# Kernel tuning notes

Hardware: AMD Instinct MI355X
Metric: run time of the kernel (lower is better)

## Reference

```python
import jax, jax.numpy as jnp
import numpy as np


def _gcn_conv(x, edge_index, edge_weight, W, b, n_nodes):
    # PyG GCNConv with normalize=True: add self-loops (weight 1), symmetric norm,
    # transform then aggregate: out[col] += norm * (x @ W)[row], plus bias.
    row = jnp.concatenate([edge_index[0], jnp.arange(n_nodes)])
    col = jnp.concatenate([edge_index[1], jnp.arange(n_nodes)])
    w = jnp.concatenate([edge_weight, jnp.ones((n_nodes,), x.dtype)])
    deg = jax.ops.segment_sum(w, col, num_segments=n_nodes)
    dinv = jnp.where(deg > 0, jax.lax.rsqrt(jnp.maximum(deg, 1e-12)), 0.0)
    norm = dinv[row] * w * dinv[col]            # [E+N]
    h = x @ W                                   # [N, out]
    msg = h[row] * norm[:, None]                # [E+N, out]
    out = jax.ops.segment_sum(msg, col, num_segments=n_nodes)
    return out + b


def setup_inputs() -> dict:
    key = jax.random.key(0)
    ks = jax.random.split(key, 6)
    N, E, F_IN, H, C = 50000, 800000, 512, 128, 40
    features = jax.random.normal(ks[0], (N, F_IN), jnp.float32)
    edge_index = jax.random.randint(ks[1], (2, E), 0, N, jnp.int64)
    edge_weight = jax.random.uniform(ks[2], (E,), jnp.float32)
    W1 = jax.random.normal(ks[3], (F_IN, H), jnp.float32) * 0.05
    b1 = jnp.zeros((H,), jnp.float32)
    W2 = jax.random.normal(ks[4], (H, C), jnp.float32) * 0.05
    b2 = jnp.zeros((C,), jnp.float32)
    return {"features": features, "edge_index": edge_index, "edge_weight": edge_weight,
            "W1": W1, "b1": b1, "W2": W2, "b2": b2}


def reference(features, edge_index, edge_weight, W1, b1, W2, b2):
    n_nodes = features.shape[0]
    x = _gcn_conv(features, edge_index, edge_weight, W1, b1, n_nodes)
    x = jax.nn.relu(x)
    # F.dropout(training=self.training): identity in eval mode
    x = _gcn_conv(x, edge_index, edge_weight, W2, b2, n_nodes)
    return jax.nn.log_softmax(x, axis=1)
```

## Files before the change

kernel.cpp:

```cpp
#include <hip/hip_runtime.h>
#include <math.h>

#define FIN  512
#define HDIM 128
#define CDIM 40
#define CPAD 48
#define CAP  64

typedef __attribute__((ext_vector_type(8))) short shortx8;
typedef __attribute__((ext_vector_type(4))) float f32x4;

__device__ inline unsigned short f2bf(float x) {
    unsigned u = __builtin_bit_cast(unsigned, x);
    unsigned r = u + 0x7fffu + ((u >> 16) & 1u);
    return (unsigned short)(r >> 16);
}
__device__ inline float bfu(unsigned short v) { return __builtin_bit_cast(float, (unsigned)v << 16); }
__device__ inline float bflo(unsigned u) { return __builtin_bit_cast(float, u << 16); }
__device__ inline float bfhi(unsigned u) { return __builtin_bit_cast(float, u & 0xffff0000u); }
__device__ inline float asf(int i) { return __builtin_bit_cast(float, i); }
__device__ inline int   asi(float f) { return __builtin_bit_cast(int, f); }

__global__ void k_fill(const int* __restrict__ row, const int* __restrict__ col,
                       const float* __restrict__ w, int* __restrict__ cursor,
                       int2* __restrict__ bkt, int E) {
    int e = blockIdx.x * blockDim.x + threadIdx.x;
    if (e >= E) return;
    const int c = col[e];
    const int p = atomicAdd(&cursor[c], 1);
    if (p < CAP) bkt[(size_t)c * CAP + p] = make_int2(row[e], asi(w[e]));
}

__global__ __launch_bounds__(256) void k_deg(const int* __restrict__ cursor,
                                             const int2* __restrict__ bkt,
                                             float* __restrict__ dinv, int n_nodes) {
    const int node = blockIdx.x * 4 + (threadIdx.x >> 6);
    const int lane = threadIdx.x & 63;
    if (node >= n_nodes) return;
    const int cnt = min(cursor[node], CAP);
    float wsum = 0.f;
    if (lane < cnt) wsum = asf(bkt[(size_t)node * CAP + lane].y);
#pragma unroll
    for (int off = 32; off; off >>= 1) wsum += __shfl_xor(wsum, off);
    if (lane == 0) dinv[node] = rsqrtf(1.0f + wsum);
}

__global__ __launch_bounds__(256) void k_norm(const int* __restrict__ cursor,
                                              int2* __restrict__ bkt,
                                              const float* __restrict__ dinv, int n_nodes) {
    const int node = blockIdx.x * 4 + (threadIdx.x >> 6);
    const int lane = threadIdx.x & 63;
    if (node >= n_nodes) return;
    const int cnt = min(cursor[node], CAP);
    const float dl = dinv[node];
    if (lane < cnt) {
        int2 pr = bkt[(size_t)node * CAP + lane];
        pr.y = asi(asf(pr.y) * dinv[pr.x] * dl);
        bkt[(size_t)node * CAP + lane] = pr;
    }
}

__global__ void k_prepw(const float* __restrict__ W1, const float* __restrict__ W2,
                        unsigned short* __restrict__ W1T, unsigned short* __restrict__ W2T) {
    const int i = blockIdx.x * blockDim.x + threadIdx.x;
    if (i < FIN * HDIM) {
        const int k = i >> 7, n = i & 127;
        W1T[n * FIN + k] = f2bf(W1[i]);
    } else {
        const int j = i - FIN * HDIM;
        if (j < CPAD * HDIM) {
            const int n = j >> 7, k = j & 127;
            W2T[j] = (n < CDIM) ? f2bf(W2[k * CDIM + n]) : (unsigned short)0;
        }
    }
}

#define G1_LDA 72
__global__ __launch_bounds__(256) void k_gemm1(const float* __restrict__ A,
                                               const unsigned short* __restrict__ W1T,
                                               unsigned short* __restrict__ h1bf, int M) {
    __shared__ short As[128 * G1_LDA];
    __shared__ short Bs[128 * G1_LDA];
    const int tid  = threadIdx.x;
    const int wave = tid >> 6;
    const int lane = tid & 63;
    const int quad = lane >> 4;
    const int mr   = lane & 15;
    const int m0w  = (wave & 1) * 64;
    const int n0w  = (wave >> 1) * 64;
    const int m0b  = blockIdx.x * 128;

    const int srow = tid >> 1;
    const int spart = tid & 1;

    f32x4 acc[4][4];
#pragma unroll
    for (int i = 0; i < 4; i++)
#pragma unroll
        for (int j = 0; j < 4; j++) acc[i][j] = (f32x4)0.f;

    const int grow = m0b + srow;
    const bool arow_ok = grow < M;
    const float* ap = A + (size_t)grow * FIN + spart * 32;
    const unsigned short* bp = W1T + (size_t)srow * FIN + spart * 32;

    for (int k0 = 0; k0 < FIN; k0 += 64) {
#pragma unroll
        for (int i = 0; i < 4; i++) {
            float4 v0 = make_float4(0.f, 0.f, 0.f, 0.f), v1 = v0;
            if (arow_ok) {
                v0 = *(const float4*)(ap + k0 + i * 8);
                v1 = *(const float4*)(ap + k0 + i * 8 + 4);
            }
            shortx8 pk;
            pk[0] = (short)f2bf(v0.x); pk[1] = (short)f2bf(v0.y);
            pk[2] = (short)f2bf(v0.z); pk[3] = (short)f2bf(v0.w);
            pk[4] = (short)f2bf(v1.x); pk[5] = (short)f2bf(v1.y);
            pk[6] = (short)f2bf(v1.z); pk[7] = (short)f2bf(v1.w);
            *(shortx8*)&As[srow * G1_LDA + spart * 32 + i * 8] = pk;
        }
#pragma unroll
        for (int i = 0; i < 4; i++)
            *(shortx8*)&Bs[srow * G1_LDA + spart * 32 + i * 8] =
                *(const shortx8*)(bp + k0 + i * 8);
        __syncthreads();

#pragma unroll
        for (int kk = 0; kk < 2; kk++) {
            shortx8 af[4], bfr[4];
#pragma unroll
            for (int mt = 0; mt < 4; mt++)
                af[mt] = *(shortx8*)&As[(m0w + mt * 16 + mr) * G1_LDA + kk * 32 + quad * 8];
#pragma unroll
            for (int nt = 0; nt < 4; nt++)
                bfr[nt] = *(shortx8*)&Bs[(n0w + nt * 16 + mr) * G1_LDA + kk * 32 + quad * 8];
#pragma unroll
            for (int mt = 0; mt < 4; mt++)
#pragma unroll
                for (int nt = 0; nt < 4; nt++)
                    acc[mt][nt] = __builtin_amdgcn_mfma_f32_16x16x32_bf16(
                        af[mt], bfr[nt], acc[mt][nt], 0, 0, 0);
        }
        __syncthreads();
    }
#pragma unroll
    for (int mt = 0; mt < 4; mt++)
#pragma unroll
        for (int r = 0; r < 4; r++) {
            const int om = m0b + m0w + mt * 16 + quad * 4 + r;
            if (om < M) {
#pragma unroll
                for (int nt = 0; nt < 4; nt++)
                    h1bf[(size_t)om * HDIM + n0w + nt * 16 + mr] = f2bf(acc[mt][nt][r]);
            }
        }
}

__global__ __launch_bounds__(256) void k_gather1(
    const int* __restrict__ cursor, const int2* __restrict__ bkt,
    const unsigned short* __restrict__ h1bf,
    const float* __restrict__ dinv, const float* __restrict__ b1,
    unsigned short* __restrict__ x1bf, int n_nodes) {
    const int node = blockIdx.x * 4 + (threadIdx.x >> 6);
    const int lane = threadIdx.x & 63;
    if (node >= n_nodes) return;
    const int cnt = min(cursor[node], CAP);
    const int2* base = bkt + (size_t)node * CAP;
    const unsigned* h32 = (const unsigned*)h1bf;
    float a0 = 0.f, a1 = 0.f;
    int s = 0;
    for (; s + 4 <= cnt; s += 4) {
        const int4 q01 = *(const int4*)(base + s);
        const int4 q23 = *(const int4*)(base + s + 2);
        const unsigned u0 = h32[(size_t)q01.x * 64 + lane];
        const unsigned u1 = h32[(size_t)q01.z * 64 + lane];
        const unsigned u2 = h32[(size_t)q23.x * 64 + lane];
        const unsigned u3 = h32[(size_t)q23.z * 64 + lane];
        const float w0 = asf(q01.y), w1 = asf(q01.w), w2 = asf(q23.y), w3 = asf(q23.w);
        a0 += w0 * bflo(u0) + w1 * bflo(u1) + w2 * bflo(u2) + w3 * bflo(u3);
        a1 += w0 * bfhi(u0) + w1 * bfhi(u1) + w2 * bfhi(u2) + w3 * bfhi(u3);
    }
    for (; s < cnt; s++) {
        const int2 pr = base[s];
        const unsigned u = h32[(size_t)pr.x * 64 + lane];
        a0 += asf(pr.y) * bflo(u);
        a1 += asf(pr.y) * bfhi(u);
    }
    const float d = dinv[node];
    const float dd = d * d;
    const unsigned us = h32[(size_t)node * 64 + lane];
    a0 = fmaxf(a0 + dd * bflo(us) + b1[lane * 2], 0.f);
    a1 = fmaxf(a1 + dd * bfhi(us) + b1[lane * 2 + 1], 0.f);
    ((unsigned*)x1bf)[(size_t)node * 64 + lane] =
        (unsigned)f2bf(a0) | ((unsigned)f2bf(a1) << 16);
}

#define G2_LDA 136
__global__ __launch_bounds__(256) void k_gemm2(const unsigned short* __restrict__ x1bf,
                                               const unsigned short* __restrict__ W2T,
                                               unsigned short* __restrict__ h2bf, int M) {
    __shared__ short Xs[128 * G2_LDA];
    __shared__ short Ws[CPAD * G2_LDA];
    const int tid  = threadIdx.x;
    const int wave = tid >> 6;
    const int lane = tid & 63;
    const int quad = lane >> 4;
    const int mr   = lane & 15;
    const int m0b  = blockIdx.x * 128;

    {
        const int srow = tid >> 1, spart = tid & 1;
        const int grow = m0b + srow;
        if (grow < M) {
            const unsigned short* xp = x1bf + (size_t)grow * HDIM + spart * 64;
#pragma unroll
            for (int i = 0; i < 8; i++)
                *(shortx8*)&Xs[srow * G2_LDA + spart * 64 + i * 8] = *(const shortx8*)(xp + i * 8);
        } else {
#pragma unroll
            for (int i = 0; i < 8; i++)
                *(shortx8*)&Xs[srow * G2_LDA + spart * 64 + i * 8] = (shortx8)0;
        }
        for (int idx = tid; idx < CPAD * 16; idx += 256) {
            const int r = idx >> 4, j = idx & 15;
            *(shortx8*)&Ws[r * G2_LDA + j * 8] = *(const shortx8*)(W2T + r * HDIM + j * 8);
        }
    }
    __syncthreads();

    f32x4 acc[2][3];
#pragma unroll
    for (int i = 0; i < 2; i++)
#pragma unroll
        for (int j = 0; j < 3; j++) acc[i][j] = (f32x4)0.f;

    const int m0w = wave * 32;
#pragma unroll
    for (int kk = 0; kk < 4; kk++) {
        shortx8 af[2], bfr[3];
#pragma unroll
        for (int mt = 0; mt < 2; mt++)
            af[mt] = *(shortx8*)&Xs[(m0w + mt * 16 + mr) * G2_LDA + kk * 32 + quad * 8];
#pragma unroll
        for (int nt = 0; nt < 3; nt++)
            bfr[nt] = *(shortx8*)&Ws[(nt * 16 + mr) * G2_LDA + kk * 32 + quad * 8];
#pragma unroll
        for (int mt = 0; mt < 2; mt++)
#pragma unroll
            for (int nt = 0; nt < 3; nt++)
                acc[mt][nt] = __builtin_amdgcn_mfma_f32_16x16x32_bf16(
                    af[mt], bfr[nt], acc[mt][nt], 0, 0, 0);
    }
#pragma unroll
    for (int mt = 0; mt < 2; mt++)
#pragma unroll
        for (int r = 0; r < 4; r++) {
            const int om = m0b + m0w + mt * 16 + quad * 4 + r;
            if (om < M) {
#pragma unroll
                for (int nt = 0; nt < 3; nt++) {
                    const int col = nt * 16 + mr;
                    if (col < CDIM)
                        h2bf[(size_t)om * CDIM + col] = f2bf(acc[mt][nt][r]);
                }
            }
        }
}

__global__ __launch_bounds__(256) void k_gather2(
    const int* __restrict__ cursor, const int2* __restrict__ bkt,
    const unsigned short* __restrict__ h2bf,
    const float* __restrict__ dinv, const float* __restrict__ b2,
    float* __restrict__ out, int n_nodes) {
    const int node = blockIdx.x * 4 + (threadIdx.x >> 6);
    const int lane = threadIdx.x & 63;
    if (node >= n_nodes) return;
    const bool act = lane < CDIM;
    const int cnt = min(cursor[node], CAP);
    const int2* base = bkt + (size_t)node * CAP;
    float acc = 0.f;
    int s = 0;
    for (; s + 4 <= cnt; s += 4) {
        const int4 q01 = *(const int4*)(base + s);
        const int4 q23 = *(const int4*)(base + s + 2);
        if (act) {
            acc += asf(q01.y) * bfu(h2bf[(size_t)q01.x * CDIM + lane])
                 + asf(q01.w) * bfu(h2bf[(size_t)q01.z * CDIM + lane])
                 + asf(q23.y) * bfu(h2bf[(size_t)q23.x * CDIM + lane])
                 + asf(q23.w) * bfu(h2bf[(size_t)q23.z * CDIM + lane]);
        }
    }
    for (; s < cnt; s++) {
        const int2 pr = base[s];
        if (act) acc += asf(pr.y) * bfu(h2bf[(size_t)pr.x * CDIM + lane]);
    }
    if (act) {
        const float d = dinv[node];
        acc += d * d * bfu(h2bf[(size_t)node * CDIM + lane]) + b2[lane];
    }
    float m = act ? acc : -INFINITY;
#pragma unroll
    for (int off = 32; off; off >>= 1) m = fmaxf(m, __shfl_xor(m, off));
    float se = act ? expf(acc - m) : 0.f;
#pragma unroll
    for (int off = 32; off; off >>= 1) se += __shfl_xor(se, off);
    if (act) out[(size_t)node * CDIM + lane] = acc - m - logf(se);
}

extern "C" void kernel_launch(void* const* d_in, const int* in_sizes, int n_in,
                              void* d_out, int out_size, void* d_ws, size_t ws_size,
                              hipStream_t stream) {
    const float* features = (const float*)d_in[0];
    const int*   eidx     = (const int*)d_in[1];
    const float* ew       = (const float*)d_in[2];
    const float* W1       = (const float*)d_in[3];
    const float* b1       = (const float*)d_in[4];
    const float* W2       = (const float*)d_in[5];
    const float* b2       = (const float*)d_in[6];
    float* out = (float*)d_out;

    const int Nn = in_sizes[0] / FIN;
    const int E  = in_sizes[2];
    const int* row = eidx;
    const int* col = eidx + E;

    char* ws = (char*)d_ws;
    size_t off = 0;
    auto alloc = [&](size_t bytes) { void* p = ws + off; off += (bytes + 255) & ~(size_t)255; return p; };
    int*   cursor          = (int*)  alloc((size_t)Nn * 4);
    float* dinv            = (float*)alloc((size_t)Nn * 4);
    int2*  bkt             = (int2*) alloc((size_t)Nn * CAP * 8);
    unsigned short* W1T    = (unsigned short*)alloc((size_t)FIN * HDIM * 2);
    unsigned short* W2T    = (unsigned short*)alloc((size_t)CPAD * HDIM * 2);
    unsigned short* h1bf   = (unsigned short*)alloc((size_t)Nn * HDIM * 2);
    unsigned short* x1bf   = (unsigned short*)alloc((size_t)Nn * HDIM * 2);
    unsigned short* h2bf   = (unsigned short*)alloc((size_t)Nn * CDIM * 2);

    hipMemsetAsync(cursor, 0, (size_t)Nn * 4, stream);
    k_fill<<<(E + 255) / 256, 256, 0, stream>>>(row, col, ew, cursor, bkt, E);
    k_deg<<<(Nn + 3) / 4, 256, 0, stream>>>(cursor, bkt, dinv, Nn);
    k_norm<<<(Nn + 3) / 4, 256, 0, stream>>>(cursor, bkt, dinv, Nn);
    const int prep_total = FIN * HDIM + CPAD * HDIM;
    k_prepw<<<(prep_total + 255) / 256, 256, 0, stream>>>(W1, W2, W1T, W2T);
    k_gemm1<<<(Nn + 127) / 128, 256, 0, stream>>>(features, W1T, h1bf, Nn);
    k_gather1<<<(Nn + 3) / 4, 256, 0, stream>>>(cursor, bkt, h1bf, dinv, b1, x1bf, Nn);
    k_gemm2<<<(Nn + 127) / 128, 256, 0, stream>>>(x1bf, W2T, h2bf, Nn);
    k_gather2<<<(Nn + 3) / 4, 256, 0, stream>>>(cursor, bkt, h2bf, dinv, b2, out, Nn);
}
```

Before: 327.1 us.

## Fold degree normalization into GEMM epilogues and packed atomic degree accumulation

Packs the edge count and a fixed-point weight sum into one 64-bit atomic per edge, so degree comes out of the fill pass and the per-node deg and norm kernels are removed. The symmetric normalization is refactored: the source-side dinv is applied in the GEMM epilogues and the destination-side dinv once per node in the gathers, so per-edge weights stay raw. Gather loops get wider unrolling with split accumulators, and h2 rows are padded to 64 elements for aligned access. The fixed-point weight sum adds small rounding error, and the 64-bit atomics may contend more than 32-bit ones.

```diff
diff --git a/kernel.cpp b/kernel.cpp
--- a/kernel.cpp
+++ b/kernel.cpp
@@ -5,6 +5,7 @@
 #define HDIM 128
 #define CDIM 40
 #define CPAD 48
+#define H2P  64
 #define CAP  64
 
 typedef __attribute__((ext_vector_type(8))) short shortx8;
@@ -22,42 +23,28 @@
 __device__ inline int   asi(float f) { return __builtin_bit_cast(int, f); }
 
 __global__ void k_fill(const int* __restrict__ row, const int* __restrict__ col,
-                       const float* __restrict__ w, int* __restrict__ cursor,
+                       const float* __restrict__ w,
+                       unsigned long long* __restrict__ cursor,
                        int2* __restrict__ bkt, int E) {
     int e = blockIdx.x * blockDim.x + threadIdx.x;
     if (e >= E) return;
     const int c = col[e];
-    const int p = atomicAdd(&cursor[c], 1);
-    if (p < CAP) bkt[(size_t)c * CAP + p] = make_int2(row[e], asi(w[e]));
-}
-
-__global__ __launch_bounds__(256) void k_deg(const int* __restrict__ cursor,
-                                             const int2* __restrict__ bkt,
-                                             float* __restrict__ dinv, int n_nodes) {
-    const int node = blockIdx.x * 4 + (threadIdx.x >> 6);
-    const int lane = threadIdx.x & 63;
-    if (node >= n_nodes) return;
-    const int cnt = min(cursor[node], CAP);
-    float wsum = 0.f;
-    if (lane < cnt) wsum = asf(bkt[(size_t)node * CAP + lane].y);
-#pragma unroll
-    for (int off = 32; off; off >>= 1) wsum += __shfl_xor(wsum, off);
-    if (lane == 0) dinv[node] = rsqrtf(1.0f + wsum);
-}
-
-__global__ __launch_bounds__(256) void k_norm(const int* __restrict__ cursor,
-                                              int2* __restrict__ bkt,
-                                              const float* __restrict__ dinv, int n_nodes) {
-    const int node = blockIdx.x * 4 + (threadIdx.x >> 6);
-    const int lane = threadIdx.x & 63;
-    if (node >= n_nodes) return;
-    const int cnt = min(cursor[node], CAP);
-    const float dl = dinv[node];
-    if (lane < cnt) {
-        int2 pr = bkt[(size_t)node * CAP + lane];
-        pr.y = asi(asf(pr.y) * dinv[pr.x] * dl);
-        bkt[(size_t)node * CAP + lane] = pr;
-    }
+    const float we = w[e];
+    const unsigned long long wfix = (unsigned long long)(we * 4294967296.0f);
+    const unsigned long long old =
+        atomicAdd(&cursor[c], (1ULL << 40) | wfix);
+    const int p = (int)(old >> 40);
+    if (p < CAP) bkt[(size_t)c * CAP + p] = make_int2(row[e], asi(we));
+}
+
+__global__ void k_deg(const unsigned long long* __restrict__ cursor,
+                      int* __restrict__ cnt, float* __restrict__ dinv, int n) {
+    const int i = blockIdx.x * blockDim.x + threadIdx.x;
+    if (i >= n) return;
+    const unsigned long long p = cursor[i];
+    cnt[i] = min((int)(p >> 40), CAP);
+    const float wsum = (float)(p & ((1ULL << 40) - 1)) * 2.3283064365386963e-10f;
+    dinv[i] = rsqrtf(1.0f + wsum);
 }
 
 __global__ void k_prepw(const float* __restrict__ W1, const float* __restrict__ W2,
@@ -78,6 +65,7 @@
 #define G1_LDA 72
 __global__ __launch_bounds__(256) void k_gemm1(const float* __restrict__ A,
                                                const unsigned short* __restrict__ W1T,
+                                               const float* __restrict__ dinv,
                                                unsigned short* __restrict__ h1bf, int M) {
     __shared__ short As[128 * G1_LDA];
     __shared__ short Bs[128 * G1_LDA];
@@ -149,48 +137,67 @@
         for (int r = 0; r < 4; r++) {
             const int om = m0b + m0w + mt * 16 + quad * 4 + r;
             if (om < M) {
+                const float dv = dinv[om];
 #pragma unroll
                 for (int nt = 0; nt < 4; nt++)
-                    h1bf[(size_t)om * HDIM + n0w + nt * 16 + mr] = f2bf(acc[mt][nt][r]);
+                    h1bf[(size_t)om * HDIM + n0w + nt * 16 + mr] = f2bf(dv * acc[mt][nt][r]);
             }
         }
 }
 
 __global__ __launch_bounds__(256) void k_gather1(
-    const int* __restrict__ cursor, const int2* __restrict__ bkt,
+    const int* __restrict__ cnt_arr, const int2* __restrict__ bkt,
     const unsigned short* __restrict__ h1bf,
     const float* __restrict__ dinv, const float* __restrict__ b1,
     unsigned short* __restrict__ x1bf, int n_nodes) {
     const int node = blockIdx.x * 4 + (threadIdx.x >> 6);
     const int lane = threadIdx.x & 63;
     if (node >= n_nodes) return;
-    const int cnt = min(cursor[node], CAP);
+    const int cnt = cnt_arr[node];
     const int2* base = bkt + (size_t)node * CAP;
     const unsigned* h32 = (const unsigned*)h1bf;
-    float a0 = 0.f, a1 = 0.f;
+    float a0 = 0.f, a1 = 0.f, c0 = 0.f, c1 = 0.f;
     int s = 0;
-    for (; s + 4 <= cnt; s += 4) {
-        const int4 q01 = *(const int4*)(base + s);
-        const int4 q23 = *(const int4*)(base + s + 2);
-        const unsigned u0 = h32[(size_t)q01.x * 64 + lane];
-        const unsigned u1 = h32[(size_t)q01.z * 64 + lane];
-        const unsigned u2 = h32[(size_t)q23.x * 64 + lane];
-        const unsigned u3 = h32[(size_t)q23.z * 64 + lane];
-        const float w0 = asf(q01.y), w1 = asf(q01.w), w2 = asf(q23.y), w3 = asf(q23.w);
-        a0 += w0 * bflo(u0) + w1 * bflo(u1) + w2 * bflo(u2) + w3 * bflo(u3);
-        a1 += w0 * bfhi(u0) + w1 * bfhi(u1) + w2 * bfhi(u2) + w3 * bfhi(u3);
-    }
-    for (; s < cnt; s++) {
+    for (; s + 8 <= cnt; s += 8) {
+        const int4 q0 = *(const int4*)(base + s);
+        const int4 q1 = *(const int4*)(base + s + 2);
+        const int4 q2 = *(const int4*)(base + s + 4);
+        const int4 q3 = *(const int4*)(base + s + 6);
+        const unsigned u0 = h32[(size_t)q0.x * 64 + lane];
+        const unsigned u1 = h32[(size_t)q0.z * 64 + lane];
+        const unsigned u2 = h32[(size_t)q1.x * 64 + lane];
+        const unsigned u3 = h32[(size_t)q1.z * 64 + lane];
+        const unsigned u4 = h32[(size_t)q2.x * 64 + lane];
+        const unsigned u5 = h32[(size_t)q2.z * 64 + lane];
+        const unsigned u6 = h32[(size_t)q3.x * 64 + lane];
+        const unsigned u7 = h32[(size_t)q3.z * 64 + lane];
+        a0 += asf(q0.y) * bflo(u0) + asf(q0.w) * bflo(u1)
+            + asf(q1.y) * bflo(u2) + asf(q1.w) * bflo(u3);
+        a1 += asf(q0.y) * bfhi(u0) + asf(q0.w) * bfhi(u1)
+            + asf(q1.y) * bfhi(u2) + asf(q1.w) * bfhi(u3);
+        c0 += asf(q2.y) * bflo(u4) + asf(q2.w) * bflo(u5)
+            + asf(q3.y) * bflo(u6) + asf(q3.w) * bflo(u7);
+        c1 += asf(q2.y) * bfhi(u4) + asf(q2.w) * bfhi(u5)
+            + asf(q3.y) * bfhi(u6) + asf(q3.w) * bfhi(u7);
+    }
+    for (; s + 2 <= cnt; s += 2) {
+        const int4 q0 = *(const int4*)(base + s);
+        const unsigned u0 = h32[(size_t)q0.x * 64 + lane];
+        const unsigned u1 = h32[(size_t)q0.z * 64 + lane];
+        a0 += asf(q0.y) * bflo(u0) + asf(q0.w) * bflo(u1);
+        a1 += asf(q0.y) * bfhi(u0) + asf(q0.w) * bfhi(u1);
+    }
+    if (s < cnt) {
         const int2 pr = base[s];
         const unsigned u = h32[(size_t)pr.x * 64 + lane];
         a0 += asf(pr.y) * bflo(u);
         a1 += asf(pr.y) * bfhi(u);
     }
-    const float d = dinv[node];
-    const float dd = d * d;
+    a0 += c0; a1 += c1;
+    const float dl = dinv[node];
     const unsigned us = h32[(size_t)node * 64 + lane];
-    a0 = fmaxf(a0 + dd * bflo(us) + b1[lane * 2], 0.f);
-    a1 = fmaxf(a1 + dd * bfhi(us) + b1[lane * 2 + 1], 0.f);
+    a0 = fmaxf(dl * (a0 + bflo(us)) + b1[lane * 2], 0.f);
+    a1 = fmaxf(dl * (a1 + bfhi(us)) + b1[lane * 2 + 1], 0.f);
     ((unsigned*)x1bf)[(size_t)node * 64 + lane] =
         (unsigned)f2bf(a0) | ((unsigned)f2bf(a1) << 16);
 }
@@ -198,6 +205,7 @@
 #define G2_LDA 136
 __global__ __launch_bounds__(256) void k_gemm2(const unsigned short* __restrict__ x1bf,
                                                const unsigned short* __restrict__ W2T,
+                                               const float* __restrict__ dinv,
                                                unsigned short* __restrict__ h2bf, int M) {
     __shared__ short Xs[128 * G2_LDA];
     __shared__ short Ws[CPAD * G2_LDA];
@@ -257,18 +265,19 @@
         for (int r = 0; r < 4; r++) {
             const int om = m0b + m0w + mt * 16 + quad * 4 + r;
             if (om < M) {
+                const float dv = dinv[om];
 #pragma unroll
                 for (int nt = 0; nt < 3; nt++) {
                     const int col = nt * 16 + mr;
                     if (col < CDIM)
-                        h2bf[(size_t)om * CDIM + col] = f2bf(acc[mt][nt][r]);
+                        h2bf[(size_t)om * H2P + col] = f2bf(dv * acc[mt][nt][r]);
                 }
             }
         }
 }
 
 __global__ __launch_bounds__(256) void k_gather2(
-    const int* __restrict__ cursor, const int2* __restrict__ bkt,
+    const int* __restrict__ cnt_arr, const int2* __restrict__ bkt,
     const unsigned short* __restrict__ h2bf,
     const float* __restrict__ dinv, const float* __restrict__ b2,
     float* __restrict__ out, int n_nodes) {
@@ -276,27 +285,28 @@
     const int lane = threadIdx.x & 63;
     if (node >= n_nodes) return;
     const bool act = lane < CDIM;
-    const int cnt = min(cursor[node], CAP);
+    const int cnt = cnt_arr[node];
     const int2* base = bkt + (size_t)node * CAP;
-    float acc = 0.f;
+    float acc = 0.f, accb = 0.f;
     int s = 0;
     for (; s + 4 <= cnt; s += 4) {
         const int4 q01 = *(const int4*)(base + s);
         const int4 q23 = *(const int4*)(base + s + 2);
         if (act) {
-            acc += asf(q01.y) * bfu(h2bf[(size_t)q01.x * CDIM + lane])
-                 + asf(q01.w) * bfu(h2bf[(size_t)q01.z * CDIM + lane])
-                 + asf(q23.y) * bfu(h2bf[(size_t)q23.x * CDIM + lane])
-                 + asf(q23.w) * bfu(h2bf[(size_t)q23.z * CDIM + lane]);
+            acc  += asf(q01.y) * bfu(h2bf[(size_t)q01.x * H2P + lane])
+                  + asf(q01.w) * bfu(h2bf[(size_t)q01.z * H2P + lane]);
+            accb += asf(q23.y) * bfu(h2bf[(size_t)q23.x * H2P + lane])
+                  + asf(q23.w) * bfu(h2bf[(size_t)q23.z * H2P + lane]);
         }
     }
     for (; s < cnt; s++) {
         const int2 pr = base[s];
-        if (act) acc += asf(pr.y) * bfu(h2bf[(size_t)pr.x * CDIM + lane]);
-    }
+        if (act) acc += asf(pr.y) * bfu(h2bf[(size_t)pr.x * H2P + lane]);
+    }
+    acc += accb;
     if (act) {
-        const float d = dinv[node];
-        acc += d * d * bfu(h2bf[(size_t)node * CDIM + lane]) + b2[lane];
+        const float dl = dinv[node];
+        acc = dl * (acc + bfu(h2bf[(size_t)node * H2P + lane])) + b2[lane];
     }
     float m = act ? acc : -INFINITY;
 #pragma unroll
@@ -327,23 +337,23 @@
     char* ws = (char*)d_ws;
     size_t off = 0;
     auto alloc = [&](size_t bytes) { void* p = ws + off; off += (bytes + 255) & ~(size_t)255; return p; };
-    int*   cursor          = (int*)  alloc((size_t)Nn * 4);
+    unsigned long long* cursor = (unsigned long long*)alloc((size_t)Nn * 8);
+    int*   cnt             = (int*)  alloc((size_t)Nn * 4);
     float* dinv            = (float*)alloc((size_t)Nn * 4);
     int2*  bkt             = (int2*) alloc((size_t)Nn * CAP * 8);
     unsigned short* W1T    = (unsigned short*)alloc((size_t)FIN * HDIM * 2);
     unsigned short* W2T    = (unsigned short*)alloc((size_t)CPAD * HDIM * 2);
     unsigned short* h1bf   = (unsigned short*)alloc((size_t)Nn * HDIM * 2);
     unsigned short* x1bf   = (unsigned short*)alloc((size_t)Nn * HDIM * 2);
-    unsigned short* h2bf   = (unsigned short*)alloc((size_t)Nn * CDIM * 2);
-
-    hipMemsetAsync(cursor, 0, (size_t)Nn * 4, stream);
+    unsigned short* h2bf   = (unsigned short*)alloc((size_t)Nn * H2P * 2);
+
+    hipMemsetAsync(cursor, 0, (size_t)Nn * 8, stream);
     k_fill<<<(E + 255) / 256, 256, 0, stream>>>(row, col, ew, cursor, bkt, E);
-    k_deg<<<(Nn + 3) / 4, 256, 0, stream>>>(cursor, bkt, dinv, Nn);
-    k_norm<<<(Nn + 3) / 4, 256, 0, stream>>>(cursor, bkt, dinv, Nn);
+    k_deg<<<(Nn + 255) / 256, 256, 0, stream>>>(cursor, cnt, dinv, Nn);
     const int prep_total = FIN * HDIM + CPAD * HDIM;
     k_prepw<<<(prep_total + 255) / 256, 256, 0, stream>>>(W1, W2, W1T, W2T);
-    k_gemm1<<<(Nn + 127) / 128, 256, 0, stream>>>(features, W1T, h1bf, Nn);
-    k_gather1<<<(Nn + 3) / 4, 256, 0, stream>>>(cursor, bkt, h1bf, dinv, b1, x1bf, Nn);
-    k_gemm2<<<(Nn + 127) / 128, 256, 0, stream>>>(x1bf, W2T, h2bf, Nn);
-    k_gather2<<<(Nn + 3) / 4, 256, 0, stream>>>(cursor, bkt, h2bf, dinv, b2, out, Nn);
-}
+    k_gemm1<<<(Nn + 127) / 128, 256, 0, stream>>>(features, W1T, dinv, h1bf, Nn);
+    k_gather1<<<(Nn + 3) / 4, 256, 0, stream>>>(cnt, bkt, h1bf, dinv, b1, x1bf, Nn);
+    k_gemm2<<<(Nn + 127) / 128, 256, 0, stream>>>(x1bf, W2T, dinv, h2bf, Nn);
+    k_gather2<<<(Nn + 3) / 4, 256, 0, stream>>>(cnt, bkt, h2bf, dinv, b2, out, Nn);
+}
```

After: 316.0 us. 3.4% less time.
